# Performance work log

Measured on AMD Instinct MI355X. Metric: run time of the kernel, lower is better.

The kernel has to match this reference:

```python
import jax, jax.numpy as jnp
import numpy as np

B, T, D_MODEL, D_STATE = 4, 4096, 1024, 256


def setup_inputs() -> dict:
    key = jax.random.key(0)
    ks = jax.random.split(key, 6)
    return {
        "x": jax.random.normal(ks[0], (B, T, D_MODEL), dtype=jnp.float32),
        "state": jnp.zeros((B, D_STATE), dtype=jnp.float32),
        "W_in": jax.random.normal(ks[1], (D_MODEL, D_STATE), dtype=jnp.float32) / np.sqrt(D_MODEL),
        "b_in": jnp.zeros((D_STATE,), dtype=jnp.float32),
        "lambda_param": jax.random.normal(ks[2], (D_STATE,), dtype=jnp.float32),
        "gamma_param": jax.random.normal(ks[3], (D_STATE,), dtype=jnp.float32),
        "W_out": jax.random.normal(ks[4], (D_STATE, D_MODEL), dtype=jnp.float32) / np.sqrt(D_STATE),
        "b_out": jnp.zeros((D_MODEL,), dtype=jnp.float32),
    }


def reference(x, state, W_in, b_in, lambda_param, gamma_param, W_out, b_out):
    # u: [B, T, d_state]
    u = jnp.einsum("btd,ds->bts", x, W_in) + b_in
    decay = jax.nn.sigmoid(lambda_param)          # [d_state]
    gu = gamma_param * u                          # [B, T, d_state]

    # linear recurrence h_t = decay * h_{t-1} + gu_t via associative scan over T
    # elements: (a, b) representing h -> a*h + b; combine: (a2*a1, a2*b1 + b2)
    a = jnp.broadcast_to(decay, gu.shape)         # [B, T, d_state]

    def combine(l, r):
        a1, b1 = l
        a2, b2 = r
        return (a2 * a1, a2 * b1 + b2)

    A, Bc = jax.lax.associative_scan(combine, (a, gu), axis=1)
    h = A * state[:, None, :] + Bc                # [B, T, d_state]

    y = jnp.einsum("bts,sd->btd", h, W_out) + b_out
    return y, h[:, -1, :]
```

## Files before the change

kernel.cpp:

```cpp
#include <hip/hip_runtime.h>
#include <hip/hip_bf16.h>
#include <math.h>

#define BB 4
#define TT 4096
#define DM 1024
#define DS 256
#define MROWS (BB*TT)

#define LCH 32
#define NCH (TT/LCH)

#define BM 128

typedef __attribute__((ext_vector_type(8))) _Float16 half8v;
typedef __attribute__((ext_vector_type(4))) float float4v;

__device__ __forceinline__ float sigmoidf_dev(float x) {
    return 1.0f / (1.0f + expf(-x));
}

__device__ __forceinline__ void gload16(const void* g, void* l) {
    __builtin_amdgcn_global_load_lds(
        (const __attribute__((address_space(1))) void*)g,
        (__attribute__((address_space(3))) void*)l, 16, 0, 0);
}

__global__ __launch_bounds__(256) void cvt_inputs(
    const float* __restrict__ x, _Float16* __restrict__ xf,
    const float* __restrict__ W1, _Float16* __restrict__ T1,
    const float* __restrict__ W2, _Float16* __restrict__ T2)
{
    if (blockIdx.x < 8192) {
        size_t u = (size_t)blockIdx.x * 256 + threadIdx.x;
        const float* p = x + u * 8;
        float4 a = *(const float4*)p;
        float4 b = *(const float4*)(p + 4);
        half8v h;
        h[0] = (_Float16)a.x; h[1] = (_Float16)a.y; h[2] = (_Float16)a.z; h[3] = (_Float16)a.w;
        h[4] = (_Float16)b.x; h[5] = (_Float16)b.y; h[6] = (_Float16)b.z; h[7] = (_Float16)b.w;
        *(half8v*)(xf + u * 8) = h;
    } else {
        const int blk = blockIdx.x - 8192;
        const int half = blk >> 10;
        int idx = (blk & 1023) * 256 + threadIdx.x;
        const float* W = half ? W2 : W1;
        _Float16* T = half ? T2 : T1;
        const int K = half ? DS : DM;
        const int N = half ? DM : DS;
        int n = idx / K, k = idx - n * K;
        T[idx] = (_Float16)W[(size_t)k * N + n];
    }
}

__global__ __launch_bounds__(256) void gemm1_fused(
    const _Float16* __restrict__ A, const _Float16* __restrict__ Bt,
    _Float16* __restrict__ gu,
    const float* __restrict__ bias, const float* __restrict__ scale,
    const float* __restrict__ lam, float* __restrict__ csum)
{
    constexpr int K = DM;
    constexpr int BN = 64, BK = 64, NF = 2, WCOLS = 32;
    constexpr int NT = K / BK;
    constexpr int BUFB = 24576;
    __shared__ char smem[3 * BUFB];

    const int nwg = gridDim.x;
    const int bid = blockIdx.x;
    const int wgid = (bid & 7) * (nwg >> 3) + (bid >> 3);
    const int GN = DS / BN;
    const int bm = wgid / GN;
    const int bn = wgid - bm * GN;

    const int tid  = threadIdx.x;
    const int lane = tid & 63;
    const int wv   = tid >> 6;
    const int wr   = wv >> 1;
    const int wc   = wv & 1;
    const int lrow = lane & 15;
    const int q16  = lane >> 4;

    float4v acc[4][NF] = {};

#define STAGE1(T, Q)                                                              \
    do {                                                                          \
        char* base_ = smem + (Q) * BUFB;                                          \
        const int k0_ = (T) * BK;                                                 \
        _Pragma("unroll")                                                         \
        for (int p = 0; p < 4; p++) {                                             \
            int c = tid + p * 256, r = c >> 3, chp = c & 7;                       \
            const _Float16* g_ = A + (size_t)(bm * BM + r) * K + k0_              \
                                   + ((chp ^ (r & 7)) << 3);                      \
            gload16(g_, base_ + c * 16);                                          \
        }                                                                         \
        _Pragma("unroll")                                                         \
        for (int p = 0; p < 2; p++) {                                             \
            int c = tid + p * 256, r = c >> 3, chp = c & 7;                       \
            const _Float16* g_ = Bt + (size_t)(bn * BN + r) * K + k0_             \
                                    + ((chp ^ (r & 7)) << 3);                     \
            gload16(g_, base_ + 16384 + c * 16);                                  \
        }                                                                         \
    } while (0)

#define COMPUTE1(Q)                                                               \
    do {                                                                          \
        char* const rb = smem + (Q) * BUFB;                                       \
        half8v a[4][2], b[NF][2];                                                 \
        _Pragma("unroll")                                                         \
        for (int i = 0; i < 4; i++) {                                             \
            int row = wr * 64 + i * 16 + lrow;                                    \
            _Pragma("unroll")                                                     \
            for (int ss = 0; ss < 2; ss++) {                                      \
                int ch = (ss * 4 + q16) ^ (row & 7);                              \
                a[i][ss] = *(const half8v*)(rb + row * 128 + ch * 16);            \
            }                                                                     \
        }                                                                         \
        _Pragma("unroll")                                                         \
        for (int j = 0; j < NF; j++) {                                            \
            int row = wc * WCOLS + j * 16 + lrow;                                 \
            _Pragma("unroll")                                                     \
            for (int ss = 0; ss < 2; ss++) {                                      \
                int ch = (ss * 4 + q16) ^ (row & 7);                              \
                b[j][ss] = *(const half8v*)(rb + 16384 + row * 128 + ch * 16);    \
            }                                                                     \
        }                                                                         \
        _Pragma("unroll")                                                         \
        for (int ss = 0; ss < 2; ss++)                                            \
            _Pragma("unroll")                                                     \
            for (int i = 0; i < 4; i++)                                           \
                _Pragma("unroll")                                                 \
                for (int j = 0; j < NF; j++)                                      \
                    acc[i][j] = __builtin_amdgcn_mfma_f32_16x16x32_f16(           \
                        a[i][ss], b[j][ss], acc[i][j], 0, 0, 0);                  \
    } while (0)

    STAGE1(0, 0);
    STAGE1(1, 1);

    int qc = 0;
    for (int t = 0; t < NT - 1; ++t) {
        asm volatile("s_waitcnt vmcnt(6)" ::: "memory");
        __builtin_amdgcn_s_barrier();
        if (t + 2 < NT) {
            int qn = qc + 2; if (qn >= 3) qn -= 3;
            STAGE1(t + 2, qn);
        }
        COMPUTE1(qc);
        qc = (qc == 2) ? 0 : qc + 1;
    }
    asm volatile("s_waitcnt vmcnt(0)" ::: "memory");
    __builtin_amdgcn_s_barrier();
    COMPUTE1(qc);
    __syncthreads();

    float* gul = (float*)smem;
#pragma unroll
    for (int j = 0; j < NF; j++) {
        int col = bn * BN + wc * WCOLS + j * 16 + lrow;
        float bi = bias[col];
        float sc = scale[col];
#pragma unroll
        for (int i = 0; i < 4; i++) {
            int r0 = bm * BM + wr * 64 + i * 16 + q16 * 4;
#pragma unroll
            for (int reg = 0; reg < 4; reg++) {
                float v = (acc[i][j][reg] + bi) * sc;
                gu[(size_t)(r0 + reg) * DS + col] = (_Float16)v;
                int lr = wr * 64 + i * 16 + q16 * 4 + reg;
                int lc = wc * WCOLS + j * 16 + lrow;
                gul[lr * 68 + lc] = v;
            }
        }
    }

    __syncthreads();
    const int lc = tid >> 6;
    const int ch = tid & 63;
    const int gcol = bn * BN + ch;
    const float d = sigmoidf_dev(lam[gcol]);
    float h = 0.0f;
#pragma unroll
    for (int rr = 0; rr < LCH; rr++)
        h = fmaf(d, h, gul[(lc * LCH + rr) * 68 + ch]);
    const int row0 = bm * BM;
    const int b    = row0 >> 12;
    const int gch  = ((row0 & 4095) >> 5) + lc;
    csum[((size_t)b * NCH + gch) * DS + gcol] = h;
#undef STAGE1
#undef COMPUTE1
}

__global__ __launch_bounds__(256) void scan_fused(
    const _Float16* __restrict__ gu, const float* __restrict__ csum,
    const float* __restrict__ state, const float* __restrict__ lam,
    _Float16* __restrict__ hf, float* __restrict__ hlast)
{
    const int s = threadIdx.x;
    const int chunk = blockIdx.x;
    const int b = blockIdx.y;
    const float d = sigmoidf_dev(lam[s]);
    float dL = d;
#pragma unroll
    for (int i = 0; i < 5; i++) dL *= dL;

    float H = state[(size_t)b * DS + s];
    const float* cp = csum + (size_t)b * NCH * DS + s;
    int k = 0;
    for (; k + 8 <= chunk; k += 8) {
        float v0 = cp[(size_t)(k + 0) * DS];
        float v1 = cp[(size_t)(k + 1) * DS];
        float v2 = cp[(size_t)(k + 2) * DS];
        float v3 = cp[(size_t)(k + 3) * DS];
        float v4 = cp[(size_t)(k + 4) * DS];
        float v5 = cp[(size_t)(k + 5) * DS];
        float v6 = cp[(size_t)(k + 6) * DS];
        float v7 = cp[(size_t)(k + 7) * DS];
        H = fmaf(dL, H, v0); H = fmaf(dL, H, v1);
        H = fmaf(dL, H, v2); H = fmaf(dL, H, v3);
        H = fmaf(dL, H, v4); H = fmaf(dL, H, v5);
        H = fmaf(dL, H, v6); H = fmaf(dL, H, v7);
    }
    for (; k < chunk; ++k)
        H = fmaf(dL, H, cp[(size_t)k * DS]);

    const size_t base = ((size_t)b * TT + (size_t)chunk * LCH) * DS + s;
    const _Float16* p = gu + base;
    _Float16* ph = hf + base;
    float h = H;
#pragma unroll
    for (int t = 0; t < LCH; t++) {
        h = fmaf(d, h, (float)p[(size_t)t * DS]);
        ph[(size_t)t * DS] = (_Float16)h;
    }
    if (chunk == NCH - 1)
        hlast[(size_t)b * DS + s] = h;
}

__global__ __launch_bounds__(256) void gemm2_f16(
    const _Float16* __restrict__ A, const _Float16* __restrict__ Bt,
    float* __restrict__ C, const float* __restrict__ bias)
{
    constexpr int BN = 128, BK = 32, NF = 4, WCOLS = 64;
    constexpr int K = DS;
    constexpr int NT = K / BK;
    constexpr int BUFB = 16384;
    __shared__ char smem[3 * BUFB];

    const int nwg = gridDim.x;
    const int bid = blockIdx.x;
    const int wgid = (bid & 7) * (nwg >> 3) + (bid >> 3);
    const int GN = DM / BN;
    const int bm = wgid / GN;
    const int bn = wgid - bm * GN;

    const int tid  = threadIdx.x;
    const int lane = tid & 63;
    const int wv   = tid >> 6;
    const int wr   = wv >> 1;
    const int wc   = wv & 1;
    const int lrow = lane & 15;
    const int q16  = lane >> 4;

    float4v acc[4][NF] = {};

#define STAGE2(T, Q)                                                              \
    do {                                                                          \
        char* base_ = smem + (Q) * BUFB;                                          \
        const int k0_ = (T) * BK;                                                 \
        _Pragma("unroll")                                                         \
        for (int p = 0; p < 2; p++) {                                             \
            int c = tid + p * 256, r = c >> 2, chp = c & 3;                       \
            const _Float16* g_ = A + (size_t)(bm * BM + r) * K + k0_              \
                                   + ((chp ^ ((r >> 1) & 3)) << 3);               \
            gload16(g_, base_ + c * 16);                                          \
        }                                                                         \
        _Pragma("unroll")                                                         \
        for (int p = 0; p < 2; p++) {                                             \
            int c = tid + p * 256, r = c >> 2, chp = c & 3;                       \
            const _Float16* g_ = Bt + (size_t)(bn * BN + r) * K + k0_             \
                                    + ((chp ^ ((r >> 1) & 3)) << 3);              \
            gload16(g_, base_ + 8192 + c * 16);                                   \
        }                                                                         \
    } while (0)

#define COMPUTE2(Q)                                                              \
    do {                                                                          \
        char* const rb = smem + (Q) * BUFB;                                       \
        half8v a[4], b[NF];                                                       \
        _Pragma("unroll")                                                         \
        for (int i = 0; i < 4; i++) {                                             \
            int row = wr * 64 + i * 16 + lrow;                                    \
            int ch = q16 ^ ((row >> 1) & 3);                                      \
            a[i] = *(const half8v*)(rb + row * 64 + ch * 16);                     \
        }                                                                         \
        _Pragma("unroll")                                                         \
        for (int j = 0; j < NF; j++) {                                            \
            int row = wc * WCOLS + j * 16 + lrow;                                 \
            int ch = q16 ^ ((row >> 1) & 3);                                      \
            b[j] = *(const half8v*)(rb + 8192 + row * 64 + ch * 16);              \
        }                                                                         \
        _Pragma("unroll")                                                         \
        for (int i = 0; i < 4; i++)                                               \
            _Pragma("unroll")                                                     \
            for (int j = 0; j < NF; j++)                                          \
                acc[i][j] = __builtin_amdgcn_mfma_f32_16x16x32_f16(               \
                    a[i], b[j], acc[i][j], 0, 0, 0);                              \
    } while (0)

    STAGE2(0, 0);
    STAGE2(1, 1);

    int qc = 0;
    for (int t = 0; t < NT - 1; ++t) {
        asm volatile("s_waitcnt vmcnt(4)" ::: "memory");
        __builtin_amdgcn_s_barrier();
        if (t + 2 < NT) {
            int qn = qc + 2; if (qn >= 3) qn -= 3;
            STAGE2(t + 2, qn);
        }
        COMPUTE2(qc);
        qc = (qc == 2) ? 0 : qc + 1;
    }
    asm volatile("s_waitcnt vmcnt(0)" ::: "memory");
    __builtin_amdgcn_s_barrier();
    COMPUTE2(qc);

#pragma unroll
    for (int j = 0; j < NF; j++) {
        int col = bn * BN + wc * WCOLS + j * 16 + lrow;
        float bi = bias[col];
#pragma unroll
        for (int i = 0; i < 4; i++) {
            int r0 = bm * BM + wr * 64 + i * 16 + q16 * 4;
#pragma unroll
            for (int reg = 0; reg < 4; reg++)
                C[(size_t)(r0 + reg) * DM + col] = acc[i][j][reg] + bi;
        }
    }
#undef STAGE2
#undef COMPUTE2
}

extern "C" void kernel_launch(void* const* d_in, const int* in_sizes, int n_in,
                              void* d_out, int out_size, void* d_ws, size_t ws_size,
                              hipStream_t stream) {
    const float* x     = (const float*)d_in[0];
    const float* state = (const float*)d_in[1];
    const float* W_in  = (const float*)d_in[2];
    const float* b_in  = (const float*)d_in[3];
    const float* lam   = (const float*)d_in[4];
    const float* gamma = (const float*)d_in[5];
    const float* W_out = (const float*)d_in[6];
    const float* b_out = (const float*)d_in[7];

    float* y     = (float*)d_out;
    float* hlast = y + (size_t)MROWS * DM;

    char* ws = (char*)d_ws;
    const size_t MB = 1024 * 1024;
    _Float16*  gu    = (_Float16*)(ws);
    float*     csum  = (float*)(ws + 8 * MB);
    _Float16*  hf    = (_Float16*)(ws + 9 * MB);
    _Float16*  w1t   = (_Float16*)(ws + 17 * MB);
    _Float16*  w2t   = (_Float16*)(ws + 17 * MB + 512 * 1024);
    _Float16*  xf    = (_Float16*)(ws + 18 * MB);

    cvt_inputs<<<dim3(10240), dim3(256), 0, stream>>>(x, xf, W_in, w1t, W_out, w2t);

    gemm1_fused<<<dim3((MROWS / BM) * (DS / 64)), dim3(256), 0, stream>>>(
        xf, w1t, gu, b_in, gamma, lam, csum);

    scan_fused<<<dim3(NCH, BB), dim3(256), 0, stream>>>(gu, csum, state, lam, hf, hlast);

    gemm2_f16<<<dim3((MROWS / BM) * (DM / 128)), dim3(256), 0, stream>>>(
        hf, w2t, y, b_out);
}
```

Baseline: 63.30 us.

## Fuse chunked scan into output GEMM via full-K A panel in LDS

Removes the separate scan kernel and its hf intermediate. Each output-GEMM block now loads its 128-row by 256 gu panel into LDS, computes the carry-in from the chunk sums, runs the recurrence in place in LDS, then streams only W_out tiles through a triple buffer. The N tile shrinks from 128 to 64 so LDS fits the full A panel, which doubles the grid. The scan is therefore recomputed by every N-tile block (16 times per row block), and the long serial carry-in loop now sits on the critical path of each GEMM block.

```diff
diff --git a/kernel.cpp b/kernel.cpp
--- a/kernel.cpp
+++ b/kernel.cpp
@@ -190,61 +190,18 @@
 #undef COMPUTE1
 }
 
-__global__ __launch_bounds__(256) void scan_fused(
+__global__ __launch_bounds__(256) void gemm2_fused(
     const _Float16* __restrict__ gu, const float* __restrict__ csum,
     const float* __restrict__ state, const float* __restrict__ lam,
-    _Float16* __restrict__ hf, float* __restrict__ hlast)
+    const _Float16* __restrict__ Bt, float* __restrict__ C,
+    const float* __restrict__ bias, float* __restrict__ hlast)
 {
-    const int s = threadIdx.x;
-    const int chunk = blockIdx.x;
-    const int b = blockIdx.y;
-    const float d = sigmoidf_dev(lam[s]);
-    float dL = d;
-#pragma unroll
-    for (int i = 0; i < 5; i++) dL *= dL;
-
-    float H = state[(size_t)b * DS + s];
-    const float* cp = csum + (size_t)b * NCH * DS + s;
-    int k = 0;
-    for (; k + 8 <= chunk; k += 8) {
-        float v0 = cp[(size_t)(k + 0) * DS];
-        float v1 = cp[(size_t)(k + 1) * DS];
-        float v2 = cp[(size_t)(k + 2) * DS];
-        float v3 = cp[(size_t)(k + 3) * DS];
-        float v4 = cp[(size_t)(k + 4) * DS];
-        float v5 = cp[(size_t)(k + 5) * DS];
-        float v6 = cp[(size_t)(k + 6) * DS];
-        float v7 = cp[(size_t)(k + 7) * DS];
-        H = fmaf(dL, H, v0); H = fmaf(dL, H, v1);
-        H = fmaf(dL, H, v2); H = fmaf(dL, H, v3);
-        H = fmaf(dL, H, v4); H = fmaf(dL, H, v5);
-        H = fmaf(dL, H, v6); H = fmaf(dL, H, v7);
-    }
-    for (; k < chunk; ++k)
-        H = fmaf(dL, H, cp[(size_t)k * DS]);
-
-    const size_t base = ((size_t)b * TT + (size_t)chunk * LCH) * DS + s;
-    const _Float16* p = gu + base;
-    _Float16* ph = hf + base;
-    float h = H;
-#pragma unroll
-    for (int t = 0; t < LCH; t++) {
-        h = fmaf(d, h, (float)p[(size_t)t * DS]);
-        ph[(size_t)t * DS] = (_Float16)h;
-    }
-    if (chunk == NCH - 1)
-        hlast[(size_t)b * DS + s] = h;
-}
-
-__global__ __launch_bounds__(256) void gemm2_f16(
-    const _Float16* __restrict__ A, const _Float16* __restrict__ Bt,
-    float* __restrict__ C, const float* __restrict__ bias)
-{
-    constexpr int BN = 128, BK = 32, NF = 4, WCOLS = 64;
+    constexpr int BN = 64, BK = 32, NF = 2, WCOLS = 32;
     constexpr int K = DS;
     constexpr int NT = K / BK;
-    constexpr int BUFB = 16384;
-    __shared__ char smem[3 * BUFB];
+    constexpr int APANEL = 65536;
+    constexpr int BBUF = 4096;
+    __shared__ char smem[APANEL + 3 * BBUF];
 
     const int nwg = gridDim.x;
     const int bid = blockIdx.x;
@@ -263,67 +220,136 @@
 
     float4v acc[4][NF] = {};
 
-#define STAGE2(T, Q)                                                              \
+#define STAGE_B2(T, Q)                                                            \
     do {                                                                          \
-        char* base_ = smem + (Q) * BUFB;                                          \
+        char* base_ = smem + APANEL + (Q) * BBUF;                                 \
         const int k0_ = (T) * BK;                                                 \
-        _Pragma("unroll")                                                         \
-        for (int p = 0; p < 2; p++) {                                             \
-            int c = tid + p * 256, r = c >> 2, chp = c & 3;                       \
-            const _Float16* g_ = A + (size_t)(bm * BM + r) * K + k0_              \
-                                   + ((chp ^ ((r >> 1) & 3)) << 3);               \
-            gload16(g_, base_ + c * 16);                                          \
-        }                                                                         \
-        _Pragma("unroll")                                                         \
-        for (int p = 0; p < 2; p++) {                                             \
-            int c = tid + p * 256, r = c >> 2, chp = c & 3;                       \
-            const _Float16* g_ = Bt + (size_t)(bn * BN + r) * K + k0_             \
-                                    + ((chp ^ ((r >> 1) & 3)) << 3);              \
-            gload16(g_, base_ + 8192 + c * 16);                                   \
-        }                                                                         \
+        int c = tid, r = c >> 2, chp = c & 3;                                     \
+        const _Float16* g_ = Bt + (size_t)(bn * BN + r) * K + k0_                 \
+                                + ((chp ^ ((r >> 1) & 3)) << 3);                  \
+        gload16(g_, base_ + c * 16);                                              \
     } while (0)
 
-#define COMPUTE2(Q)                                                              \
-    do {                                                                          \
-        char* const rb = smem + (Q) * BUFB;                                       \
-        half8v a[4], b[NF];                                                       \
-        _Pragma("unroll")                                                         \
-        for (int i = 0; i < 4; i++) {                                             \
-            int row = wr * 64 + i * 16 + lrow;                                    \
-            int ch = q16 ^ ((row >> 1) & 3);                                      \
-            a[i] = *(const half8v*)(rb + row * 64 + ch * 16);                     \
-        }                                                                         \
-        _Pragma("unroll")                                                         \
-        for (int j = 0; j < NF; j++) {                                            \
-            int row = wc * WCOLS + j * 16 + lrow;                                 \
-            int ch = q16 ^ ((row >> 1) & 3);                                      \
-            b[j] = *(const half8v*)(rb + 8192 + row * 64 + ch * 16);              \
-        }                                                                         \
-        _Pragma("unroll")                                                         \
-        for (int i = 0; i < 4; i++)                                               \
-            _Pragma("unroll")                                                     \
-            for (int j = 0; j < NF; j++)                                          \
-                acc[i][j] = __builtin_amdgcn_mfma_f32_16x16x32_f16(               \
-                    a[i], b[j], acc[i][j], 0, 0, 0);                              \
-    } while (0)
-
-    STAGE2(0, 0);
-    STAGE2(1, 1);
+    STAGE_B2(0, 0);
+    STAGE_B2(1, 1);
+#pragma unroll
+    for (int p = 0; p < 16; p++) {
+        int c = tid + p * 256;
+        int r = c >> 5, ch = c & 31;
+        const _Float16* g_ = gu + (size_t)(bm * BM + r) * K + ((ch ^ (r & 7)) << 3);
+        gload16(g_, smem + c * 16);
+    }
+    asm volatile("s_waitcnt vmcnt(0)" ::: "memory");
+    __builtin_amdgcn_s_barrier();
+
+    {
+        const int s = tid;
+        const float d = sigmoidf_dev(lam[s]);
+        float dL = d;
+#pragma unroll
+        for (int i = 0; i < 5; i++) dL *= dL;
+        const int row0 = bm * BM;
+        const int b    = row0 >> 12;
+        const int lcb  = (row0 & 4095) >> 5;
+        float H = state[(size_t)b * DS + s];
+        const float* cp = csum + (size_t)b * NCH * DS + s;
+        int k = 0;
+        for (; k + 8 <= lcb; k += 8) {
+            float v0 = cp[(size_t)(k + 0) * DS];
+            float v1 = cp[(size_t)(k + 1) * DS];
+            float v2 = cp[(size_t)(k + 2) * DS];
+            float v3 = cp[(size_t)(k + 3) * DS];
+            float v4 = cp[(size_t)(k + 4) * DS];
+            float v5 = cp[(size_t)(k + 5) * DS];
+            float v6 = cp[(size_t)(k + 6) * DS];
+            float v7 = cp[(size_t)(k + 7) * DS];
+            H = fmaf(dL, H, v0); H = fmaf(dL, H, v1);
+            H = fmaf(dL, H, v2); H = fmaf(dL, H, v3);
+            H = fmaf(dL, H, v4); H = fmaf(dL, H, v5);
+            H = fmaf(dL, H, v6); H = fmaf(dL, H, v7);
+        }
+        for (; k < lcb; ++k)
+            H = fmaf(dL, H, cp[(size_t)k * DS]);
+
+        float h = H;
+        for (int t = 0; t < BM; t += 8) {
+            float v[8];
+#pragma unroll
+            for (int u = 0; u < 8; u++) {
+                int tt = t + u;
+                v[u] = (float)*(const _Float16*)(smem + tt * 512 +
+                         (((s >> 3) ^ (tt & 7)) << 4) + ((s & 7) << 1));
+            }
+#pragma unroll
+            for (int u = 0; u < 8; u++) {
+                int tt = t + u;
+                h = fmaf(d, h, v[u]);
+                *(_Float16*)(smem + tt * 512 +
+                    (((s >> 3) ^ (tt & 7)) << 4) + ((s & 7) << 1)) = (_Float16)h;
+            }
+        }
+        if (((bm & 31) == 31) && bn == 0)
+            hlast[(size_t)b * DS + s] = h;
+    }
+    __syncthreads();
 
     int qc = 0;
     for (int t = 0; t < NT - 1; ++t) {
-        asm volatile("s_waitcnt vmcnt(4)" ::: "memory");
+        asm volatile("s_waitcnt vmcnt(1)" ::: "memory");
         __builtin_amdgcn_s_barrier();
         if (t + 2 < NT) {
             int qn = qc + 2; if (qn >= 3) qn -= 3;
-            STAGE2(t + 2, qn);
-        }
-        COMPUTE2(qc);
+            STAGE_B2(t + 2, qn);
+        }
+        {
+            char* const bb = smem + APANEL + qc * BBUF;
+            half8v a[4], b[NF];
+#pragma unroll
+            for (int i = 0; i < 4; i++) {
+                int row = wr * 64 + i * 16 + lrow;
+                int ch = (t * 4 + q16) ^ (row & 7);
+                a[i] = *(const half8v*)(smem + row * 512 + ch * 16);
+            }
+#pragma unroll
+            for (int j = 0; j < NF; j++) {
+                int row = wc * WCOLS + j * 16 + lrow;
+                int ch = q16 ^ ((row >> 1) & 3);
+                b[j] = *(const half8v*)(bb + row * 64 + ch * 16);
+            }
+#pragma unroll
+            for (int i = 0; i < 4; i++)
+#pragma unroll
+                for (int j = 0; j < NF; j++)
+                    acc[i][j] = __builtin_amdgcn_mfma_f32_16x16x32_f16(
+                        a[i], b[j], acc[i][j], 0, 0, 0);
+        }
         qc = (qc == 2) ? 0 : qc + 1;
     }
     asm volatile("s_waitcnt vmcnt(0)" ::: "memory");
     __builtin_amdgcn_s_barrier();
-    COMPUTE2(qc);
+    {
+        const int t = NT - 1;
+        char* const bb = smem + APANEL + qc * BBUF;
+        half8v a[4], b[NF];
+#pragma unroll
+        for (int i = 0; i < 4; i++) {
+            int row = wr * 64 + i * 16 + lrow;
+            int ch = (t * 4 + q16) ^ (row & 7);
+            a[i] = *(const half8v*)(smem + row * 512 + ch * 16);
+        }
+#pragma unroll
+        for (int j = 0; j < NF; j++) {
+            int row = wc * WCOLS + j * 16 + lrow;
+            int ch = q16 ^ ((row >> 1) & 3);
+            b[j] = *(const half8v*)(bb + row * 64 + ch * 16);
+        }
+#pragma unroll
+        for (int i = 0; i < 4; i++)
+#pragma unroll
+            for (int j = 0; j < NF; j++)
+                acc[i][j] = __builtin_amdgcn_mfma_f32_16x16x32_f16(
+                    a[i], b[j], acc[i][j], 0, 0, 0);
+    }
 
 #pragma unroll
     for (int j = 0; j < NF; j++) {
@@ -337,8 +363,7 @@
                 C[(size_t)(r0 + reg) * DM + col] = acc[i][j][reg] + bi;
         }
     }
-#undef STAGE2
-#undef COMPUTE2
+#undef STAGE_B2
 }
 
 extern "C" void kernel_launch(void* const* d_in, const int* in_sizes, int n_in,
@@ -360,18 +385,15 @@
     const size_t MB = 1024 * 1024;
     _Float16*  gu    = (_Float16*)(ws);
     float*     csum  = (float*)(ws + 8 * MB);
-    _Float16*  hf    = (_Float16*)(ws + 9 * MB);
-    _Float16*  w1t   = (_Float16*)(ws + 17 * MB);
-    _Float16*  w2t   = (_Float16*)(ws + 17 * MB + 512 * 1024);
-    _Float16*  xf    = (_Float16*)(ws + 18 * MB);
+    _Float16*  w1t   = (_Float16*)(ws + 9 * MB);
+    _Float16*  w2t   = (_Float16*)(ws + 9 * MB + 512 * 1024);
+    _Float16*  xf    = (_Float16*)(ws + 10 * MB);
 
     cvt_inputs<<<dim3(10240), dim3(256), 0, stream>>>(x, xf, W_in, w1t, W_out, w2t);
 
     gemm1_fused<<<dim3((MROWS / BM) * (DS / 64)), dim3(256), 0, stream>>>(
         xf, w1t, gu, b_in, gamma, lam, csum);
 
-    scan_fused<<<dim3(NCH, BB), dim3(256), 0, stream>>>(gu, csum, state, lam, hf, hlast);
-
-    gemm2_f16<<<dim3((MROWS / BM) * (DM / 128)), dim3(256), 0, stream>>>(
-        hf, w2t, y, b_out);
-}
+    gemm2_fused<<<dim3((MROWS / BM) * (DM / 64)), dim3(256), 0, stream>>>(
+        gu, csum, state, lam, w2t, y, b_out, hlast);
+}
```

New measurement: 78.82 us. 24.5% more time.
